# Kernel tuning notes

Measured on AMD Instinct MI355X. Metric: run time of the kernel, lower is better.

Reference implementation:

```python
import jax, jax.numpy as jnp
import numpy as np

K = 64          # num_clusters
S = 4           # num_shadow
DIM = 128
ALPHA = 100.0
EPS = 1e-12     # F.normalize eps


def setup_inputs() -> dict:
    key = jax.random.key(0)
    k1, k2 = jax.random.split(key)
    x = jax.random.normal(k1, (16, DIM, 30, 40), dtype=jnp.float32)
    centroids = jax.random.uniform(k2, (K, S + 1, DIM), dtype=jnp.float32)
    return {"x": x, "centroids": centroids}


def reference(x, centroids):
    N, C, H, W = x.shape
    P = H * W
    # conv weight/bias derived from centroids (as in _init_params)
    c_flat = centroids.reshape(K * (S + 1), C)                      # (M, C)
    w = 2.0 * ALPHA * c_flat                                        # (M, C)
    b = -ALPHA * jnp.linalg.norm(c_flat, axis=1)                    # (M,)
    xf = x.reshape(N, C, P)                                         # (N, C, P)
    # 1x1 conv == per-pixel matmul
    conv_out = jnp.einsum('ncp,mc->nmp', xf, w) + b[None, :, None]
    conv_out = conv_out.reshape(N, K, S + 1, P)
    # dual softmax: over clusters (axis=1) and over shadows (axis=2)
    soft_assign = jax.nn.softmax(conv_out, axis=1) * jax.nn.softmax(conv_out, axis=2)
    # loop `residual += sa_i * residual` == residual0 * prod_i(1 + sa_i)
    mult = jnp.prod(1.0 + soft_assign, axis=2)                      # (N, K, P)
    rep = centroids[:, 0, :]                                        # (K, C) representative centroids
    # sum_p mult * (x - rep) without materializing (N,K,C,P)
    out = jnp.einsum('ncp,nkp->nkc', xf, mult) \
          - rep[None, :, :] * jnp.sum(mult, axis=-1)[:, :, None]    # (N, K, C)
    # intra-cluster L2 norm (per descriptor dim)
    out = out / jnp.maximum(jnp.linalg.norm(out, axis=2, keepdims=True), EPS)
    out = out.reshape(N, -1)
    # global L2 norm
    out = out / jnp.maximum(jnp.linalg.norm(out, axis=1, keepdims=True), EPS)
    return out
```

## Files before the change

### kernel.cpp

```cpp
#include <hip/hip_runtime.h>
#include <math.h>

typedef _Float16 f16;
typedef unsigned short u16;
typedef unsigned int u32;
typedef f16 f16x8 __attribute__((ext_vector_type(8)));
typedef float f32x4 __attribute__((ext_vector_type(4)));

namespace {
constexpr int Kc  = 64;
constexpr int SP1 = 5;
constexpr int Mm  = Kc * SP1;
constexpr int DIM = 128;
constexpr int Nn  = 16;
constexpr int Pp  = 1200;
constexpr int PT  = 64;
constexpr int NT  = (Pp + PT - 1) / PT;
constexpr int WAVES = 16;
constexpr int TPB   = WAVES * 64;
constexpr int KPW   = Kc / WAVES;

constexpr int OFF_A    = 0;
constexpr int OFF_BH   = 87040;
constexpr int OFF_BL   = 104448;
constexpr int OFF_PART = 121856;
constexpr int OFF_M1F  = 142336;
constexpr int OFF_Z1F  = 143616;
constexpr int OFF_MS   = 144896;
constexpr int OFF_BS   = 154112;
constexpr int LDS_TOTAL = 155392;
}

__global__ __launch_bounds__(256) void k_bias(const float* __restrict__ cent,
                                              float* __restrict__ b) {
  const int w = threadIdx.x >> 6, lane = threadIdx.x & 63;
  const int m = blockIdx.x * 4 + w;
  const float* r = cent + (size_t)m * DIM;
  float s = r[lane] * r[lane] + r[lane + 64] * r[lane + 64];
  #pragma unroll
  for (int off = 32; off > 0; off >>= 1) s += __shfl_down(s, off, 64);
  if (lane == 0) b[m] = -100.0f * sqrtf(s);
}

__global__ __launch_bounds__(1024) void k_prep_cent(
    const float* __restrict__ cent, u16* __restrict__ Ah, u16* __restrict__ Al) {
  const int i = blockIdx.x * 1024 + threadIdx.x;
  const float v = cent[i];
  const f16 h  = (f16)v;
  const f16 lo = (f16)(v - (float)h);
  Ah[i] = __builtin_bit_cast(u16, h);
  Al[i] = __builtin_bit_cast(u16, lo);
}

__global__ __launch_bounds__(256) void k_prep_x(
    const float* __restrict__ x, u16* __restrict__ xh_t, u16* __restrict__ xl_t) {
  const int tile = blockIdx.x, n = blockIdx.y;
  const int p0 = tile * PT, cnt = min(PT, Pp - p0);
  __shared__ float ls[PT][DIM + 1];
  for (int i = threadIdx.x; i < DIM * PT; i += 256) {
    const int c = i >> 6, p = i & 63;
    ls[p][c] = (p < cnt) ? x[((size_t)n * DIM + c) * Pp + p0 + p] : 0.f;
  }
  __syncthreads();
  for (int i = threadIdx.x; i < PT * DIM; i += 256) {
    const int p = i >> 7, c = i & 127;
    if (p < cnt) {
      const float v = ls[p][c];
      const f16 h  = (f16)v;
      const f16 lo = (f16)(v - (float)h);
      const size_t o = ((size_t)n * Pp + p0 + p) * DIM + c;
      xh_t[o] = __builtin_bit_cast(u16, h);
      xl_t[o] = __builtin_bit_cast(u16, lo);
    }
  }
}

__global__ __launch_bounds__(TPB, 4) void k_fused(
    const float* __restrict__ x, const u16* __restrict__ Ah_g,
    const u16* __restrict__ Al_g, const u16* __restrict__ xh_t,
    const u16* __restrict__ xl_t, const float* __restrict__ b_g,
    float* __restrict__ out_acc, float* __restrict__ S_part) {
  const int tile = blockIdx.x, n = blockIdx.y;
  const int p0 = tile * PT, cnt = min(PT, Pp - p0);
  const int t = threadIdx.x, lane = t & 63, w = t >> 6;
  const int l15 = lane & 15, g = lane >> 4;
  const bool act = lane < cnt;

  extern __shared__ __align__(16) char smem[];
  f16*   Ablk   = (f16*)(smem + OFF_A);
  f16*   Bh_s   = (f16*)(smem + OFF_BH);
  f16*   Bl_s   = (f16*)(smem + OFF_BL);
  float* part   = (float*)(smem + OFF_PART);
  float* m1f    = (float*)(smem + OFF_M1F);
  float* z1f    = (float*)(smem + OFF_Z1F);
  f16*   mult_s = (f16*)(smem + OFF_MS);
  float* b_s    = (float*)(smem + OFF_BS);
  float* convs  = (float*)(smem + OFF_A);
  f16*   xpv    = (f16*)(smem + OFF_A);

  for (int i2 = t; i2 < Mm * DIM / 2; i2 += TPB) {
    const int m = i2 >> 6, c2 = i2 & 63;
    *(u32*)&Ablk[m * 136 + c2 * 2] = ((const u32*)Ah_g)[i2];
  }
  for (int i2 = t; i2 < PT * DIM / 2; i2 += TPB) {
    const int p = i2 >> 6, c2 = i2 & 63;
    const u32 vh = (p < cnt) ? ((const u32*)xh_t)[((size_t)n * Pp + p0 + p) * 64 + c2] : 0u;
    const u32 vl = (p < cnt) ? ((const u32*)xl_t)[((size_t)n * Pp + p0 + p) * 64 + c2] : 0u;
    *(u32*)&Bh_s[p * 136 + c2 * 2] = vh;
    *(u32*)&Bl_s[p * 136 + c2 * 2] = vl;
  }
  if (t < Mm) b_s[t] = b_g[t];
  __syncthreads();

  const int wm = w >> 2, wp = w & 3;
  const int m0 = wm * 80;
  f32x4 acc[5];
  #pragma unroll
  for (int i = 0; i < 5; ++i) acc[i] = (f32x4){0.f, 0.f, 0.f, 0.f};

  #pragma unroll
  for (int seg = 0; seg < 3; ++seg) {
    if (seg == 2) {
      __syncthreads();
      for (int i2 = t; i2 < Mm * DIM / 2; i2 += TPB) {
        const int m = i2 >> 6, c2 = i2 & 63;
        *(u32*)&Ablk[m * 136 + c2 * 2] = ((const u32*)Al_g)[i2];
      }
      __syncthreads();
    }
    const f16* Bseg = (seg == 1) ? Bl_s : Bh_s;
    #pragma unroll
    for (int kc = 0; kc < 4; ++kc) {
      const f16x8 bf = *(const f16x8*)&Bseg[(wp * 16 + l15) * 136 + kc * 32 + g * 8];
      #pragma unroll
      for (int t5 = 0; t5 < 5; ++t5) {
        const f16x8 af = *(const f16x8*)&Ablk[(m0 + t5 * 16 + l15) * 136 + kc * 32 + g * 8];
        acc[t5] = __builtin_amdgcn_mfma_f32_16x16x32_f16(af, bf, acc[t5], 0, 0, 0);
      }
    }
  }
  __syncthreads();

  const int pcol = wp * 16 + l15;
  #pragma unroll
  for (int t5 = 0; t5 < 5; ++t5)
    #pragma unroll
    for (int r = 0; r < 4; ++r) {
      const int m = m0 + t5 * 16 + g * 4 + r;
      convs[m * 64 + pcol] = fmaf(200.0f, acc[t5][r], b_s[m]);
    }
  __syncthreads();

  float cv[KPW][SP1];
  float m1loc[SP1];
  #pragma unroll
  for (int s = 0; s < SP1; ++s) m1loc[s] = -3.4e38f;
  #pragma unroll
  for (int kk = 0; kk < KPW; ++kk)
    #pragma unroll
    for (int s = 0; s < SP1; ++s) {
      const float v = convs[((w * KPW + kk) * SP1 + s) * 64 + lane];
      cv[kk][s] = v;
      m1loc[s] = fmaxf(m1loc[s], v);
    }
  __syncthreads();

  for (int i = t; i < DIM * PT; i += TPB) {
    const int c = i >> 6, p = i & 63;
    const float v = (p < cnt) ? x[((size_t)n * DIM + c) * Pp + p0 + p] : 0.f;
    xpv[c * 72 + p] = (f16)v;
  }

  #pragma unroll
  for (int s = 0; s < SP1; ++s) part[(w * SP1 + s) * 64 + lane] = m1loc[s];
  __syncthreads();
  if (t < SP1 * 64) {
    const int s = t >> 6, l = t & 63;
    float m = part[s * 64 + l];
    #pragma unroll
    for (int ww = 1; ww < WAVES; ++ww) m = fmaxf(m, part[(ww * SP1 + s) * 64 + l]);
    m1f[s * 64 + l] = m;
  }
  __syncthreads();
  float m1r[SP1];
  #pragma unroll
  for (int s = 0; s < SP1; ++s) m1r[s] = m1f[s * 64 + lane];
  float z1loc[SP1] = {0.f, 0.f, 0.f, 0.f, 0.f};
  #pragma unroll
  for (int kk = 0; kk < KPW; ++kk)
    #pragma unroll
    for (int s = 0; s < SP1; ++s) z1loc[s] += __expf(cv[kk][s] - m1r[s]);
  #pragma unroll
  for (int s = 0; s < SP1; ++s) part[(w * SP1 + s) * 64 + lane] = z1loc[s];
  __syncthreads();
  if (t < SP1 * 64) {
    const int s = t >> 6, l = t & 63;
    float z = part[s * 64 + l];
    #pragma unroll
    for (int ww = 1; ww < WAVES; ++ww) z += part[(ww * SP1 + s) * 64 + l];
    z1f[s * 64 + l] = z;
  }
  __syncthreads();
  float z1r[SP1];
  #pragma unroll
  for (int s = 0; s < SP1; ++s) z1r[s] = z1f[s * 64 + lane];

  #pragma unroll
  for (int kk = 0; kk < KPW; ++kk) {
    const int k = w * KPW + kk;
    float M2 = cv[kk][0];
    #pragma unroll
    for (int s = 1; s < SP1; ++s) M2 = fmaxf(M2, cv[kk][s]);
    float e2[SP1], Z2 = 0.f;
    #pragma unroll
    for (int s = 0; s < SP1; ++s) { e2[s] = __expf(cv[kk][s] - M2); Z2 += e2[s]; }
    float mlt = 1.f;
    #pragma unroll
    for (int s = 0; s < SP1; ++s) {
      const float e1 = __expf(cv[kk][s] - m1r[s]);
      mlt *= 1.f + (e1 / z1r[s]) * (e2[s] / Z2);
    }
    mult_s[k * 72 + lane] = act ? (f16)mlt : (f16)0.f;
    float msum = act ? mlt : 0.f;
    #pragma unroll
    for (int off = 32; off > 0; off >>= 1) msum += __shfl_down(msum, off, 64);
    if (lane == 0) S_part[((size_t)n * NT + tile) * Kc + k] = msum;
  }
  __syncthreads();

  const int wm2 = w & 3;
  const int wn2 = (w >> 2) * 2;
  f32x4 acc2[2];
  acc2[0] = (f32x4){0.f, 0.f, 0.f, 0.f};
  acc2[1] = (f32x4){0.f, 0.f, 0.f, 0.f};
  #pragma unroll
  for (int kc = 0; kc < 2; ++kc) {
    const f16x8 am = *(const f16x8*)&mult_s[(wm2 * 16 + l15) * 72 + kc * 32 + g * 8];
    #pragma unroll
    for (int tn = 0; tn < 2; ++tn) {
      const f16x8 bx = *(const f16x8*)&xpv[((wn2 + tn) * 16 + l15) * 72 + kc * 32 + g * 8];
      acc2[tn] = __builtin_amdgcn_mfma_f32_16x16x32_f16(am, bx, acc2[tn], 0, 0, 0);
    }
  }
  #pragma unroll
  for (int tn = 0; tn < 2; ++tn)
    #pragma unroll
    for (int r = 0; r < 4; ++r) {
      const int k = wm2 * 16 + g * 4 + r;
      const int c = (wn2 + tn) * 16 + l15;
      atomicAdd(&out_acc[((size_t)n * Kc + k) * DIM + c], acc2[tn][r]);
    }
}

__global__ __launch_bounds__(256) void k_norm(
    const float* __restrict__ out_acc, const float* __restrict__ cent,
    const float* __restrict__ S_part, float* __restrict__ out) {
  const int n = blockIdx.y, k0 = blockIdx.x * 8;
  __shared__ float Sk[8];
  if (threadIdx.x < 8) {
    float s = 0.f;
    for (int tt = 0; tt < NT; ++tt)
      s += S_part[((size_t)n * NT + tt) * Kc + k0 + threadIdx.x];
    Sk[threadIdx.x] = s;
  }
  __syncthreads();
  const int kl = threadIdx.x >> 5, cl = threadIdx.x & 31;
  const int k = k0 + kl;
  const float sk = Sk[kl];
  float v[4], ss = 0.f;
  #pragma unroll
  for (int j = 0; j < 4; ++j) {
    const int c = cl + 32 * j;
    v[j] = out_acc[((size_t)n * Kc + k) * DIM + c]
         - cent[(size_t)k * SP1 * DIM + c] * sk;
    ss = fmaf(v[j], v[j], ss);
  }
  #pragma unroll
  for (int off = 16; off > 0; off >>= 1) ss += __shfl_xor(ss, off, 32);
  const float kinv = 0.125f / fmaxf(sqrtf(ss), 1e-12f);
  #pragma unroll
  for (int j = 0; j < 4; ++j)
    out[((size_t)n * Kc + k) * DIM + cl + 32 * j] = v[j] * kinv;
}

extern "C" void kernel_launch(void* const* d_in, const int* in_sizes, int n_in,
                              void* d_out, int out_size, void* d_ws, size_t ws_size,
                              hipStream_t stream) {
  const float* x    = (const float*)d_in[0];
  const float* cent = (const float*)d_in[1];
  float* out = (float*)d_out;

  float* b       = (float*)d_ws;
  float* S_part  = b + 384;
  float* out_acc = S_part + (size_t)Nn * NT * Kc;
  u16* Ah_g = (u16*)(out_acc + (size_t)Nn * Kc * DIM);
  u16* Al_g = Ah_g + (size_t)Mm * DIM;
  u16* xh_t = Al_g + (size_t)Mm * DIM;
  u16* xl_t = xh_t + (size_t)Nn * Pp * DIM;

  hipMemsetAsync(out_acc, 0, (size_t)Nn * Kc * DIM * sizeof(float), stream);
  k_bias<<<dim3(Mm / 4), dim3(256), 0, stream>>>(cent, b);
  k_prep_cent<<<dim3(Mm * DIM / 1024), dim3(1024), 0, stream>>>(cent, Ah_g, Al_g);
  k_prep_x<<<dim3(NT, Nn), dim3(256), 0, stream>>>(x, xh_t, xl_t);
  k_fused<<<dim3(NT, Nn), dim3(TPB), LDS_TOTAL, stream>>>(
      x, Ah_g, Al_g, xh_t, xl_t, b, out_acc, S_part);
  k_norm<<<dim3(8, Nn), dim3(256), 0, stream>>>(out_acc, cent, S_part, out);
}
```

Measured before the change: 144.0 us.

## Fuse x fp16 split into main kernel, merge prep kernels, replace atomics with partials

The separate k_prep_x pass is removed. x is now loaded once per tile into LDS scratch, where it is split into hi/lo fp16 and transposed. The hi copy is reused for the second GEMM instead of re-reading x from global memory. The bias and centroid-split kernels are merged into one launch. The memset and per-element atomics are replaced by per-tile partial outputs that k_norm sums, which cuts launches and global traffic but adds a larger workspace and a serial NT-long reduction in the norm kernel.

```diff
diff --git a/kernel.cpp b/kernel.cpp
--- a/kernel.cpp
+++ b/kernel.cpp
@@ -31,55 +31,28 @@
 constexpr int LDS_TOTAL = 155392;
 }
 
-__global__ __launch_bounds__(256) void k_bias(const float* __restrict__ cent,
-                                              float* __restrict__ b) {
+__global__ __launch_bounds__(1024) void k_prep(
+    const float* __restrict__ cent, float* __restrict__ b,
+    u16* __restrict__ Ah, u16* __restrict__ Al) {
   const int w = threadIdx.x >> 6, lane = threadIdx.x & 63;
-  const int m = blockIdx.x * 4 + w;
-  const float* r = cent + (size_t)m * DIM;
-  float s = r[lane] * r[lane] + r[lane + 64] * r[lane + 64];
+  const int m = blockIdx.x * 16 + w;
+  const float v0 = cent[(size_t)m * DIM + lane];
+  const float v1 = cent[(size_t)m * DIM + 64 + lane];
+  float s = v0 * v0 + v1 * v1;
   #pragma unroll
   for (int off = 32; off > 0; off >>= 1) s += __shfl_down(s, off, 64);
   if (lane == 0) b[m] = -100.0f * sqrtf(s);
-}
-
-__global__ __launch_bounds__(1024) void k_prep_cent(
-    const float* __restrict__ cent, u16* __restrict__ Ah, u16* __restrict__ Al) {
-  const int i = blockIdx.x * 1024 + threadIdx.x;
-  const float v = cent[i];
-  const f16 h  = (f16)v;
-  const f16 lo = (f16)(v - (float)h);
-  Ah[i] = __builtin_bit_cast(u16, h);
-  Al[i] = __builtin_bit_cast(u16, lo);
-}
-
-__global__ __launch_bounds__(256) void k_prep_x(
-    const float* __restrict__ x, u16* __restrict__ xh_t, u16* __restrict__ xl_t) {
-  const int tile = blockIdx.x, n = blockIdx.y;
-  const int p0 = tile * PT, cnt = min(PT, Pp - p0);
-  __shared__ float ls[PT][DIM + 1];
-  for (int i = threadIdx.x; i < DIM * PT; i += 256) {
-    const int c = i >> 6, p = i & 63;
-    ls[p][c] = (p < cnt) ? x[((size_t)n * DIM + c) * Pp + p0 + p] : 0.f;
-  }
-  __syncthreads();
-  for (int i = threadIdx.x; i < PT * DIM; i += 256) {
-    const int p = i >> 7, c = i & 127;
-    if (p < cnt) {
-      const float v = ls[p][c];
-      const f16 h  = (f16)v;
-      const f16 lo = (f16)(v - (float)h);
-      const size_t o = ((size_t)n * Pp + p0 + p) * DIM + c;
-      xh_t[o] = __builtin_bit_cast(u16, h);
-      xl_t[o] = __builtin_bit_cast(u16, lo);
-    }
-  }
+  const f16 h0 = (f16)v0, h1 = (f16)v1;
+  Ah[(size_t)m * DIM + lane]      = __builtin_bit_cast(u16, h0);
+  Ah[(size_t)m * DIM + 64 + lane] = __builtin_bit_cast(u16, h1);
+  Al[(size_t)m * DIM + lane]      = __builtin_bit_cast(u16, (f16)(v0 - (float)h0));
+  Al[(size_t)m * DIM + 64 + lane] = __builtin_bit_cast(u16, (f16)(v1 - (float)h1));
 }
 
 __global__ __launch_bounds__(TPB, 4) void k_fused(
     const float* __restrict__ x, const u16* __restrict__ Ah_g,
-    const u16* __restrict__ Al_g, const u16* __restrict__ xh_t,
-    const u16* __restrict__ xl_t, const float* __restrict__ b_g,
-    float* __restrict__ out_acc, float* __restrict__ S_part) {
+    const u16* __restrict__ Al_g, const float* __restrict__ b_g,
+    float* __restrict__ out_part, float* __restrict__ S_part) {
   const int tile = blockIdx.x, n = blockIdx.y;
   const int p0 = tile * PT, cnt = min(PT, Pp - p0);
   const int t = threadIdx.x, lane = t & 63, w = t >> 6;
@@ -87,29 +60,42 @@
   const bool act = lane < cnt;
 
   extern __shared__ __align__(16) char smem[];
-  f16*   Ablk   = (f16*)(smem + OFF_A);
-  f16*   Bh_s   = (f16*)(smem + OFF_BH);
-  f16*   Bl_s   = (f16*)(smem + OFF_BL);
-  float* part   = (float*)(smem + OFF_PART);
-  float* m1f    = (float*)(smem + OFF_M1F);
-  float* z1f    = (float*)(smem + OFF_Z1F);
-  f16*   mult_s = (f16*)(smem + OFF_MS);
-  float* b_s    = (float*)(smem + OFF_BS);
-  float* convs  = (float*)(smem + OFF_A);
-  f16*   xpv    = (f16*)(smem + OFF_A);
+  f16*   Ablk    = (f16*)(smem + OFF_A);
+  u32*   Ablk32  = (u32*)(smem + OFF_A);
+  f16*   Bh_s    = (f16*)(smem + OFF_BH);
+  u32*   Bh32    = (u32*)(smem + OFF_BH);
+  f16*   Bl_s    = (f16*)(smem + OFF_BL);
+  u32*   Bl32    = (u32*)(smem + OFF_BL);
+  float* part    = (float*)(smem + OFF_PART);
+  float* scratch = (float*)(smem + OFF_PART);
+  float* m1f     = (float*)(smem + OFF_M1F);
+  float* z1f     = (float*)(smem + OFF_Z1F);
+  f16*   mult_s  = (f16*)(smem + OFF_MS);
+  float* b_s     = (float*)(smem + OFF_BS);
+  float* convs   = (float*)(smem + OFF_A);
+  u16*   xpv     = (u16*)(smem + OFF_A);
 
   for (int i2 = t; i2 < Mm * DIM / 2; i2 += TPB) {
     const int m = i2 >> 6, c2 = i2 & 63;
-    *(u32*)&Ablk[m * 136 + c2 * 2] = ((const u32*)Ah_g)[i2];
-  }
-  for (int i2 = t; i2 < PT * DIM / 2; i2 += TPB) {
-    const int p = i2 >> 6, c2 = i2 & 63;
-    const u32 vh = (p < cnt) ? ((const u32*)xh_t)[((size_t)n * Pp + p0 + p) * 64 + c2] : 0u;
-    const u32 vl = (p < cnt) ? ((const u32*)xl_t)[((size_t)n * Pp + p0 + p) * 64 + c2] : 0u;
-    *(u32*)&Bh_s[p * 136 + c2 * 2] = vh;
-    *(u32*)&Bl_s[p * 136 + c2 * 2] = vl;
-  }
-  if (t < Mm) b_s[t] = b_g[t];
+    Ablk32[m * 68 + c2] = ((const u32*)Ah_g)[i2];
+  }
+  for (int i = t; i < DIM * PT; i += TPB) {
+    const int c = i >> 6, p = i & 63;
+    scratch[p * 129 + c] = (p < cnt) ? x[((size_t)n * DIM + c) * Pp + p0 + p] : 0.f;
+  }
+  __syncthreads();
+
+  for (int i = t; i < PT * 64; i += TPB) {
+    const int p = i >> 6, c2 = i & 63;
+    const float v0 = scratch[p * 129 + 2 * c2];
+    const float v1 = scratch[p * 129 + 2 * c2 + 1];
+    const f16 h0 = (f16)v0, h1 = (f16)v1;
+    const f16 l0 = (f16)(v0 - (float)h0), l1 = (f16)(v1 - (float)h1);
+    Bh32[p * 68 + c2] = (u32)__builtin_bit_cast(u16, h0) |
+                        ((u32)__builtin_bit_cast(u16, h1) << 16);
+    Bl32[p * 68 + c2] = (u32)__builtin_bit_cast(u16, l0) |
+                        ((u32)__builtin_bit_cast(u16, l1) << 16);
+  }
   __syncthreads();
 
   const int wm = w >> 2, wp = w & 3;
@@ -124,8 +110,9 @@
       __syncthreads();
       for (int i2 = t; i2 < Mm * DIM / 2; i2 += TPB) {
         const int m = i2 >> 6, c2 = i2 & 63;
-        *(u32*)&Ablk[m * 136 + c2 * 2] = ((const u32*)Al_g)[i2];
+        Ablk32[m * 68 + c2] = ((const u32*)Al_g)[i2];
       }
+      if (t < Mm) b_s[t] = b_g[t];
       __syncthreads();
     }
     const f16* Bseg = (seg == 1) ? Bl_s : Bh_s;
@@ -167,8 +154,7 @@
 
   for (int i = t; i < DIM * PT; i += TPB) {
     const int c = i >> 6, p = i & 63;
-    const float v = (p < cnt) ? x[((size_t)n * DIM + c) * Pp + p0 + p] : 0.f;
-    xpv[c * 72 + p] = (f16)v;
+    xpv[c * 72 + p] = ((const u16*)Bh_s)[p * 136 + c];
   }
 
   #pragma unroll
@@ -238,49 +224,49 @@
     const f16x8 am = *(const f16x8*)&mult_s[(wm2 * 16 + l15) * 72 + kc * 32 + g * 8];
     #pragma unroll
     for (int tn = 0; tn < 2; ++tn) {
-      const f16x8 bx = *(const f16x8*)&xpv[((wn2 + tn) * 16 + l15) * 72 + kc * 32 + g * 8];
+      const f16x8 bx = *(const f16x8*)((const f16*)xpv + ((wn2 + tn) * 16 + l15) * 72 + kc * 32 + g * 8);
       acc2[tn] = __builtin_amdgcn_mfma_f32_16x16x32_f16(am, bx, acc2[tn], 0, 0, 0);
     }
   }
+  float* dst = out_part + ((size_t)(n * NT + tile) * Kc) * DIM;
   #pragma unroll
   for (int tn = 0; tn < 2; ++tn)
     #pragma unroll
-    for (int r = 0; r < 4; ++r) {
-      const int k = wm2 * 16 + g * 4 + r;
-      const int c = (wn2 + tn) * 16 + l15;
-      atomicAdd(&out_acc[((size_t)n * Kc + k) * DIM + c], acc2[tn][r]);
-    }
+    for (int r = 0; r < 4; ++r)
+      dst[(wm2 * 16 + g * 4 + r) * DIM + (wn2 + tn) * 16 + l15] = acc2[tn][r];
 }
 
 __global__ __launch_bounds__(256) void k_norm(
-    const float* __restrict__ out_acc, const float* __restrict__ cent,
+    const float* __restrict__ out_part, const float* __restrict__ cent,
     const float* __restrict__ S_part, float* __restrict__ out) {
-  const int n = blockIdx.y, k0 = blockIdx.x * 8;
-  __shared__ float Sk[8];
-  if (threadIdx.x < 8) {
+  const int n = blockIdx.y, k0 = blockIdx.x * 4;
+  __shared__ float Sk[4];
+  if (threadIdx.x < 4) {
     float s = 0.f;
     for (int tt = 0; tt < NT; ++tt)
       s += S_part[((size_t)n * NT + tt) * Kc + k0 + threadIdx.x];
     Sk[threadIdx.x] = s;
   }
   __syncthreads();
-  const int kl = threadIdx.x >> 5, cl = threadIdx.x & 31;
+  const int kl = threadIdx.x >> 6, cl = threadIdx.x & 63;
   const int k = k0 + kl;
   const float sk = Sk[kl];
-  float v[4], ss = 0.f;
-  #pragma unroll
-  for (int j = 0; j < 4; ++j) {
-    const int c = cl + 32 * j;
-    v[j] = out_acc[((size_t)n * Kc + k) * DIM + c]
-         - cent[(size_t)k * SP1 * DIM + c] * sk;
+  float v[2], ss = 0.f;
+  #pragma unroll
+  for (int j = 0; j < 2; ++j) {
+    const int c = cl + 64 * j;
+    float a = 0.f;
+    for (int tt = 0; tt < NT; ++tt)
+      a += out_part[(((size_t)n * NT + tt) * Kc + k) * DIM + c];
+    v[j] = a - cent[(size_t)k * SP1 * DIM + c] * sk;
     ss = fmaf(v[j], v[j], ss);
   }
   #pragma unroll
-  for (int off = 16; off > 0; off >>= 1) ss += __shfl_xor(ss, off, 32);
+  for (int off = 32; off > 0; off >>= 1) ss += __shfl_xor(ss, off, 64);
   const float kinv = 0.125f / fmaxf(sqrtf(ss), 1e-12f);
   #pragma unroll
-  for (int j = 0; j < 4; ++j)
-    out[((size_t)n * Kc + k) * DIM + cl + 32 * j] = v[j] * kinv;
+  for (int j = 0; j < 2; ++j)
+    out[((size_t)n * Kc + k) * DIM + cl + 64 * j] = v[j] * kinv;
 }
 
 extern "C" void kernel_launch(void* const* d_in, const int* in_sizes, int n_in,
@@ -290,19 +276,14 @@
   const float* cent = (const float*)d_in[1];
   float* out = (float*)d_out;
 
-  float* b       = (float*)d_ws;
-  float* S_part  = b + 384;
-  float* out_acc = S_part + (size_t)Nn * NT * Kc;
-  u16* Ah_g = (u16*)(out_acc + (size_t)Nn * Kc * DIM);
+  float* b        = (float*)d_ws;
+  float* S_part   = b + 384;
+  float* out_part = S_part + (size_t)Nn * NT * Kc;
+  u16* Ah_g = (u16*)(out_part + (size_t)Nn * NT * Kc * DIM);
   u16* Al_g = Ah_g + (size_t)Mm * DIM;
-  u16* xh_t = Al_g + (size_t)Mm * DIM;
-  u16* xl_t = xh_t + (size_t)Nn * Pp * DIM;
-
-  hipMemsetAsync(out_acc, 0, (size_t)Nn * Kc * DIM * sizeof(float), stream);
-  k_bias<<<dim3(Mm / 4), dim3(256), 0, stream>>>(cent, b);
-  k_prep_cent<<<dim3(Mm * DIM / 1024), dim3(1024), 0, stream>>>(cent, Ah_g, Al_g);
-  k_prep_x<<<dim3(NT, Nn), dim3(256), 0, stream>>>(x, xh_t, xl_t);
+
+  k_prep<<<dim3(Mm / 16), dim3(1024), 0, stream>>>(cent, b, Ah_g, Al_g);
   k_fused<<<dim3(NT, Nn), dim3(TPB), LDS_TOTAL, stream>>>(
-      x, Ah_g, Al_g, xh_t, xl_t, b, out_acc, S_part);
-  k_norm<<<dim3(8, Nn), dim3(256), 0, stream>>>(out_acc, cent, S_part, out);
-}
+      x, Ah_g, Al_g, b, out_part, S_part);
+  k_norm<<<dim3(Kc / 4, Nn), dim3(256), 0, stream>>>(out_part, cent, S_part, out);
+}
```

New measurement: 117.0 us. 18.7% less time.
